# Optimization experiments

Measured on AMD Instinct MI355X. Metric: run time of the kernel, lower is better.

## Reference

```python
import jax, jax.numpy as jnp
import numpy as np
from jax import lax

N_EMBED, N_HEAD, N_EXPERTS, TOP_K = 1024, 16, 8, 2
D_FF = 4 * N_EMBED
HEAD = N_EMBED // N_HEAD
LN_EPS = 1e-5


def _layernorm(x, gamma, beta):
    mu = jnp.mean(x, axis=-1, keepdims=True)
    var = jnp.var(x, axis=-1, keepdims=True)
    return (x - mu) * lax.rsqrt(var + LN_EPS) * gamma + beta


def setup_inputs() -> dict:
    key = jax.random.key(0)
    ks = jax.random.split(key, 16)
    B, T = 2, 2048
    s = 0.02
    return {
        "x": jax.random.normal(ks[0], (B, T, N_EMBED), jnp.float32),
        "noise": jax.random.normal(ks[1], (B, T, N_EXPERTS), jnp.float32),
        "gamma1": jnp.ones((N_EMBED,), jnp.float32),
        "beta1": jnp.zeros((N_EMBED,), jnp.float32),
        "gamma2": jnp.ones((N_EMBED,), jnp.float32),
        "beta2": jnp.zeros((N_EMBED,), jnp.float32),
        "w_qkv": jax.random.normal(ks[2], (N_EMBED, 3 * N_EMBED), jnp.float32) * s,
        "w_out": jax.random.normal(ks[3], (N_EMBED, N_EMBED), jnp.float32) * s,
        "w_route": jax.random.normal(ks[4], (N_EMBED, N_EXPERTS), jnp.float32) * s,
        "b_route": jnp.zeros((N_EXPERTS,), jnp.float32),
        "w_noise": jax.random.normal(ks[5], (N_EMBED, N_EXPERTS), jnp.float32) * s,
        "b_noise": jnp.zeros((N_EXPERTS,), jnp.float32),
        "w1": jax.random.normal(ks[6], (N_EXPERTS, N_EMBED, D_FF), jnp.float32) * s,
        "b1": jnp.zeros((N_EXPERTS, D_FF), jnp.float32),
        "w2": jax.random.normal(ks[7], (N_EXPERTS, D_FF, N_EMBED), jnp.float32) * s,
        "b2": jnp.zeros((N_EXPERTS, N_EMBED), jnp.float32),
    }


def _attention(h, w_qkv, w_out):
    B, T, C = h.shape
    qkv = (h @ w_qkv).reshape(B, T, 3, N_HEAD, HEAD)
    q, k, v = qkv[:, :, 0], qkv[:, :, 1], qkv[:, :, 2]  # (B,T,H,hd)
    scores = jnp.einsum("bthd,bshd->bhts", q, k) / jnp.sqrt(jnp.float32(HEAD))
    attn = jax.nn.softmax(scores, axis=-1)
    out = jnp.einsum("bhts,bshd->bthd", attn, v)  # (B,T,H,hd)
    # faithful reproduction of the original permute/reshape/permute sequence
    out = jnp.transpose(out, (0, 2, 1, 3)).reshape(B, C, T)
    out = jnp.transpose(out, (0, 2, 1))  # (B,T,C)
    return out @ w_out


def _sparse_moe(h, noise, w_route, b_route, w_noise, b_noise, w1, b1, w2, b2):
    B, T, C = h.shape
    N = B * T
    flat = h.reshape(N, C)
    logits = flat @ w_route + b_route
    noise_logits = flat @ w_noise + b_noise
    noisy = logits + noise.reshape(N, N_EXPERTS) * jax.nn.softplus(noise_logits)
    full_probs = jax.nn.softmax(noisy, axis=-1)
    top_vals, top_idx = lax.top_k(noisy, TOP_K)  # (N,k)
    gates = jax.nn.softmax(top_vals, axis=-1)
    dense_gates = jnp.zeros((N, N_EXPERTS), flat.dtype).at[
        jnp.arange(N)[:, None], top_idx
    ].set(gates)
    cap = (N * TOP_K) // N_EXPERTS  # expert capacity, capacity_factor=1.0
    updates = jnp.zeros_like(flat)
    for i in range(N_EXPERTS):
        mask = (top_idx == i).any(axis=-1)  # (N,)
        order = jnp.argsort((~mask).astype(jnp.int32), stable=True)
        idx = order[:cap]
        valid = mask[idx]
        xi = flat[idx]  # (cap,C)
        hid = jax.nn.relu(xi @ w1[i] + b1[i])
        yo = hid @ w2[i] + b2[i]
        g = dense_gates[idx, i] * valid.astype(flat.dtype)
        updates = updates.at[idx].add(yo * g[:, None])
    moe_out = updates.reshape(B, T, C)
    entropy = -jnp.sum(full_probs * jnp.log(full_probs + 1e-8), axis=-1)
    return moe_out, entropy.mean()


def reference(x, noise, gamma1, beta1, gamma2, beta2, w_qkv, w_out,
              w_route, b_route, w_noise, b_noise, w1, b1, w2, b2):
    x = x + _attention(_layernorm(x, gamma1, beta1), w_qkv, w_out)
    moe_out, entropy_loss = _sparse_moe(_layernorm(x, gamma2, beta2), noise,
                                        w_route, b_route, w_noise, b_noise,
                                        w1, b1, w2, b2)
    return x + moe_out, entropy_loss
```

## Files before the change

kernel.cpp:

```cpp
#include <hip/hip_runtime.h>
#include <hip/hip_bf16.h>


#define TT   2048
#define NTOK 4096
#define CE   1024
#define DFF  4096
#define NE   8
#define CAP  1024

typedef __bf16 bf16;
typedef __attribute__((ext_vector_type(8))) bf16 bf16x8;
typedef __attribute__((ext_vector_type(4))) bf16 bf16x4;
typedef __attribute__((ext_vector_type(4))) float f32x4;

typedef __attribute__((address_space(1))) const void* as1_t;
typedef __attribute__((address_space(3))) void* as3_t;
__device__ __forceinline__ void gll16(const void* g, void* l) {
  __builtin_amdgcn_global_load_lds((as1_t)g, (as3_t)l, 16, 0, 0);
}

__device__ __forceinline__ void split2(float v, bf16& h, bf16& l) {
  h = (bf16)v;
  l = (bf16)(v - (float)h);
}

template <bool LO>
__global__ __launch_bounds__(256) void wsplit_k(const float* __restrict__ W,
                                                bf16* __restrict__ Th,
                                                bf16* __restrict__ Tl,
                                                int K, int N, long sW, long sT) {
  __shared__ float tile[64][65];
  const int e = blockIdx.z;
  const float* Wb = W + (long)e * sW;
  bf16* Thb = Th + (long)e * sT;
  bf16* Tlb = LO ? Tl + (long)e * sT : nullptr;
  const int k0 = blockIdx.y * 64, n0 = blockIdx.x * 64;
  const int tx = threadIdx.x & 15, ty = threadIdx.x >> 4;
#pragma unroll
  for (int i = 0; i < 4; i++) {
    int kk = ty + i * 16;
    float4 v = *(const float4*)&Wb[(long)(k0 + kk) * N + n0 + tx * 4];
    tile[kk][tx * 4 + 0] = v.x;
    tile[kk][tx * 4 + 1] = v.y;
    tile[kk][tx * 4 + 2] = v.z;
    tile[kk][tx * 4 + 3] = v.w;
  }
  __syncthreads();
#pragma unroll
  for (int i = 0; i < 4; i++) {
    int nn = ty + i * 16;
    bf16x4 hv, lv;
#pragma unroll
    for (int j = 0; j < 4; j++) {
      float v = tile[tx * 4 + j][nn];
      bf16 h, l;
      split2(v, h, l);
      hv[j] = h;
      lv[j] = l;
    }
    long o = (long)(n0 + nn) * K + k0 + tx * 4;
    *(bf16x4*)(Thb + o) = hv;
    if (LO) *(bf16x4*)(Tlb + o) = lv;
  }
}

__global__ __launch_bounds__(256) void vsplit_k(const float* __restrict__ V,
                                                bf16* __restrict__ Th,
                                                bf16* __restrict__ Tl) {
  __shared__ float tile[64][65];
  const int b = blockIdx.z;
  const int vd0 = blockIdx.x * 64, t0 = blockIdx.y * 64;
  const int tx = threadIdx.x & 15, ty = threadIdx.x >> 4;
#pragma unroll
  for (int i = 0; i < 4; i++) {
    int tt = ty + i * 16;
    float4 v = *(const float4*)&V[((long)b * TT + t0 + tt) * 1024 + vd0 + tx * 4];
    tile[tt][tx * 4 + 0] = v.x;
    tile[tt][tx * 4 + 1] = v.y;
    tile[tt][tx * 4 + 2] = v.z;
    tile[tt][tx * 4 + 3] = v.w;
  }
  __syncthreads();
#pragma unroll
  for (int i = 0; i < 4; i++) {
    int vd = ty + i * 16;
    bf16x4 hv, lv;
#pragma unroll
    for (int j = 0; j < 4; j++) {
      float v = tile[tx * 4 + j][vd];
      bf16 h, l;
      split2(v, h, l);
      hv[j] = h;
      lv[j] = l;
    }
    long o = ((long)b * 1024 + vd0 + vd) * (long)TT + t0 + tx * 4;
    *(bf16x4*)(Th + o) = hv;
    *(bf16x4*)(Tl + o) = lv;
  }
}

__global__ __launch_bounds__(256) void ln_k(const float* __restrict__ in,
                                            const float* __restrict__ g,
                                            const float* __restrict__ b,
                                            float* __restrict__ outf,
                                            bf16* __restrict__ outh,
                                            bf16* __restrict__ outl,
                                            float* __restrict__ zp) {
  int row = blockIdx.x, tid = threadIdx.x;
  if (zp && row == 0 && tid < 64) zp[tid] = 0.f;
  const float* xr = in + (long)row * CE;
  float v[4];
  float s = 0.f, s2 = 0.f;
#pragma unroll
  for (int i = 0; i < 4; i++) {
    v[i] = xr[tid + 256 * i];
    s += v[i];
    s2 += v[i] * v[i];
  }
#pragma unroll
  for (int o = 32; o; o >>= 1) {
    s += __shfl_xor(s, o);
    s2 += __shfl_xor(s2, o);
  }
  __shared__ float rs[4], rs2[4];
  int w = tid >> 6, lane = tid & 63;
  if (lane == 0) { rs[w] = s; rs2[w] = s2; }
  __syncthreads();
  s = rs[0] + rs[1] + rs[2] + rs[3];
  s2 = rs2[0] + rs2[1] + rs2[2] + rs2[3];
  float mu = s * (1.f / CE);
  float var = s2 * (1.f / CE) - mu * mu;
  float rstd = rsqrtf(var + 1e-5f);
  long rb = (long)row * CE;
#pragma unroll
  for (int i = 0; i < 4; i++) {
    int c = tid + 256 * i;
    float y = (v[i] - mu) * rstd * g[c] + b[c];
    if (outf) outf[rb + c] = y;
    bf16 h, l;
    split2(y, h, l);
    outh[rb + c] = h;
    outl[rb + c] = l;
  }
}

template <int NPASS, int EPI, bool AGATHER, int TM>
__global__ __launch_bounds__(256, 2) void gemm_k(
    const bf16* __restrict__ Ah, const bf16* __restrict__ Al,
    const bf16* __restrict__ BTh, const bf16* __restrict__ BTl,
    void* __restrict__ O0, void* __restrict__ O1, void* __restrict__ O2,
    int M, int N, int K, const float* __restrict__ resid,
    const float* __restrict__ bias, const int* __restrict__ tokens,
    const int* __restrict__ counts, const float* __restrict__ gslot,
    long sA, long sBT, long sC, int sBias, const bf16* __restrict__ zp) {
  constexpr int NS = (NPASS > 1) ? 2 : 1;
  constexpr int MI = TM / 32;
  constexpr int AISS = TM / 64;
  __shared__ bf16 As[NS][TM * 32];
  __shared__ bf16 Bs[NS][128 * 32];
  const int e = blockIdx.z;
  const int n0 = blockIdx.x * 128, m0 = blockIdx.y * TM;
  const int tid = threadIdx.x;
  const int w = tid >> 6, lane = tid & 63, lm = lane & 15, qd = lane >> 4;
  const int wm = (w & 1) * (TM / 2), wn = (w >> 1) * 64;

  const bf16* Ab = Ah + (long)e * sA;
  const bf16* AbL = (NS > 1) ? Al + (long)e * sA : nullptr;
  const bf16* Bb = BTh + (long)e * sBT;
  const bf16* BbL = (NS > 1) ? BTl + (long)e * sBT : nullptr;

  const int kc = (lane & 3) * 8;
  int cnt = 0;
  if (AGATHER || EPI == 3) cnt = counts[e];

  const bf16* aP[AISS];
  const bf16* aPL[AISS];
  int aStep[AISS];
  int ldsA[AISS];
#pragma unroll
  for (int ii = 0; ii < AISS; ii++) {
    int sr = w * (TM / 4) + ii * 16 + (lane >> 2);
    ldsA[ii] = (w * TM + ii * 64) * 8;
    aStep[ii] = 32;
    if (AGATHER) {
      int gm = m0 + sr;
      int tk = (gm < cnt) ? tokens[e * CAP + gm] : -1;
      if (tk < 0) { aP[ii] = (const bf16*)zp + kc; aStep[ii] = 0; }
      else aP[ii] = Ab + (long)tk * K + kc;
    } else {
      aP[ii] = Ab + (long)(m0 + sr) * K + kc;
    }
    aPL[ii] = (NS > 1) ? AbL + (aP[ii] - Ab) : nullptr;
  }
  const bf16* bP[2];
  const bf16* bPL[2];
  int ldsB[2];
#pragma unroll
  for (int ii = 0; ii < 2; ii++) {
    int sr = w * 32 + ii * 16 + (lane >> 2);
    ldsB[ii] = (w * 128 + ii * 64) * 8;
    bP[ii] = Bb + (long)(n0 + sr) * K + kc;
    bPL[ii] = (NS > 1) ? BbL + (bP[ii] - Bb) : nullptr;
  }

  f32x4 acc[MI][4];
#pragma unroll
  for (int i = 0; i < MI; i++)
#pragma unroll
    for (int j = 0; j < 4; j++) acc[i][j] = (f32x4){0.f, 0.f, 0.f, 0.f};

  for (int k0 = 0; k0 < K; k0 += 32) {
#pragma unroll
    for (int ii = 0; ii < AISS; ii++) {
      gll16(aP[ii], (char*)&As[0][0] + ldsA[ii] * 2);
      if (NS > 1) gll16(aPL[ii], (char*)&As[1][0] + ldsA[ii] * 2);
      aP[ii] += aStep[ii];
      if (NS > 1) aPL[ii] += aStep[ii];
    }
#pragma unroll
    for (int ii = 0; ii < 2; ii++) {
      gll16(bP[ii], (char*)&Bs[0][0] + ldsB[ii] * 2);
      if (NS > 1) gll16(bPL[ii], (char*)&Bs[1][0] + ldsB[ii] * 2);
      bP[ii] += 32;
      if (NS > 1) bPL[ii] += 32;
    }
    __syncthreads();
    bf16x8 af[NS][MI], bfv[NS][4];
#pragma unroll
    for (int j = 0; j < 4; j++)
#pragma unroll
      for (int s = 0; s < NS; s++)
        bfv[s][j] = *(const bf16x8*)&Bs[s][(wn + j * 16 + lm) * 32 + qd * 8];
#pragma unroll
    for (int i = 0; i < MI; i++)
#pragma unroll
      for (int s = 0; s < NS; s++)
        af[s][i] = *(const bf16x8*)&As[s][(wm + i * 16 + lm) * 32 + qd * 8];
#pragma unroll
    for (int i = 0; i < MI; i++)
#pragma unroll
      for (int j = 0; j < 4; j++) {
        acc[i][j] = __builtin_amdgcn_mfma_f32_16x16x32_bf16(
            af[0][i], bfv[0][j], acc[i][j], 0, 0, 0);
        if (NPASS > 1) {
          acc[i][j] = __builtin_amdgcn_mfma_f32_16x16x32_bf16(
              af[0][i], bfv[1][j], acc[i][j], 0, 0, 0);
          acc[i][j] = __builtin_amdgcn_mfma_f32_16x16x32_bf16(
              af[1][i], bfv[0][j], acc[i][j], 0, 0, 0);
        }
      }
    __syncthreads();
  }
#pragma unroll
  for (int i = 0; i < MI; i++)
#pragma unroll
    for (int j = 0; j < 4; j++) {
      long row = m0 + wm + i * 16 + qd * 4;
      long col = n0 + wn + j * 16 + lm;
      if (EPI == 0) {
        if (col < 2048) {
          bf16* qh = (bf16*)O0;
          bf16* ql = (bf16*)O1;
#pragma unroll
          for (int r = 0; r < 4; r++) {
            bf16 h, l;
            split2(acc[i][j][r], h, l);
            qh[(row + r) * 2048 + col] = h;
            ql[(row + r) * 2048 + col] = l;
          }
        } else {
          float* vt = (float*)O2;
          long vd = col - 2048;
#pragma unroll
          for (int r = 0; r < 4; r++) vt[(row + r) * 1024 + vd] = acc[i][j][r];
        }
      } else if (EPI == 1) {
        float* outp = (float*)O0;
#pragma unroll
        for (int r = 0; r < 4; r++)
          outp[(row + r) * N + col] = resid[(row + r) * N + col] + acc[i][j][r];
      } else if (EPI == 2) {
        bf16* hid = (bf16*)O0;
        float bv = bias[e * sBias + col];
#pragma unroll
        for (int r = 0; r < 4; r++) {
          float t = acc[i][j][r] + bv;
          hid[(long)e * sC + (row + r) * (long)N + col] =
              (bf16)(t > 0.f ? t : 0.f);
        }
      } else {
        float* outp = (float*)O0;
        float bv = bias[e * sBias + col];
#pragma unroll
        for (int r = 0; r < 4; r++) {
          long rr = row + r;
          if (rr < cnt) {
            int tok = tokens[e * CAP + rr];
            float gv = gslot[e * CAP + rr];
            atomicAdd(&outp[(long)tok * CE + col], gv * (acc[i][j][r] + bv));
          }
        }
      }
    }
}

__global__ __launch_bounds__(512, 4) void attn_k(
    const bf16* __restrict__ qkvh, const bf16* __restrict__ qkvl,
    const bf16* __restrict__ VTh, const bf16* __restrict__ VTl,
    bf16* __restrict__ attn_h, bf16* __restrict__ attn_l) {
  const int qt = blockIdx.x, h = blockIdx.y, b = blockIdx.z;
  const int tid = threadIdx.x, w = tid >> 6, lane = tid & 63;
  const int lm = lane & 15, qd = lane >> 4;
  __shared__ bf16 Ks[2][64 * 64];
  __shared__ bf16 Vs[2][64 * 64];
  __shared__ bf16 Ps[8][2][16][40];
  const long bb = (long)b * TT;

  bf16x8 qfh[2], qfl[2];
  {
    long qrow = (bb + qt * 128 + w * 16 + lm) * 2048 + h * 64;
#pragma unroll
    for (int kk = 0; kk < 2; kk++) {
      qfh[kk] = *(const bf16x8*)(qkvh + qrow + kk * 32 + qd * 8);
      qfl[kk] = *(const bf16x8*)(qkvl + qrow + kk * 32 + qd * 8);
    }
  }

  const int ktok = tid >> 3, dc = tid & 7;
  const int kws = ktok * 64 + ((dc ^ (ktok & 7)) * 8);
  const long gK0 = (bb + ktok) * 2048 + 1024 + h * 64 + dc * 8;
  const int vd = tid >> 3, tc = tid & 7;
  const int vws = vd * 64 + ((tc ^ (vd & 7)) * 8);
  const long gV0 = ((long)b * 1024 + h * 64 + vd) * (long)TT + tc * 8;

  const bf16* pKh = qkvh + gK0;
  const bf16* pKl = qkvl + gK0;
  const bf16* pVh = VTh + gV0;
  const bf16* pVl = VTl + gV0;

  float4 rkh, rkl, rvh, rvl;
#define LOADT()                  \
  do {                           \
    rkh = *(const float4*)(pKh); \
    rkl = *(const float4*)(pKl); \
    rvh = *(const float4*)(pVh); \
    rvl = *(const float4*)(pVl); \
  } while (0)
  LOADT();

  float l_lane[4];
  f32x4 o[4];
#pragma unroll
  for (int r = 0; r < 4; r++) l_lane[r] = 0.f;
#pragma unroll
  for (int nt = 0; nt < 4; nt++) o[nt] = (f32x4){0.f, 0.f, 0.f, 0.f};

  const float SC = 0.125f * 1.4426950408889634f;

  for (int kt = 0; kt < TT / 64; kt++) {
    __syncthreads();
    *(float4*)&Ks[0][kws] = rkh;
    *(float4*)&Ks[1][kws] = rkl;
    *(float4*)&Vs[0][vws] = rvh;
    *(float4*)&Vs[1][vws] = rvl;
    if (kt != TT / 64 - 1) {
      pKh += 64 * 2048; pKl += 64 * 2048; pVh += 64; pVl += 64;
      LOADT();
    }
    __syncthreads();
#pragma unroll
    for (int th = 0; th < 2; th++) {
      f32x4 sv[2];
#pragma unroll
      for (int ntl = 0; ntl < 2; ntl++) sv[ntl] = (f32x4){0.f, 0.f, 0.f, 0.f};
#pragma unroll
      for (int ntl = 0; ntl < 2; ntl++) {
        int tok = (th * 2 + ntl) * 16 + lm;
#pragma unroll
        for (int kk = 0; kk < 2; kk++) {
          int slot = ((kk * 4 + qd) ^ (lm & 7)) * 8;
          bf16x8 kh = *(const bf16x8*)&Ks[0][tok * 64 + slot];
          bf16x8 kl = *(const bf16x8*)&Ks[1][tok * 64 + slot];
          sv[ntl] = __builtin_amdgcn_mfma_f32_16x16x32_bf16(qfh[kk], kh,
                                                            sv[ntl], 0, 0, 0);
          sv[ntl] = __builtin_amdgcn_mfma_f32_16x16x32_bf16(qfh[kk], kl,
                                                            sv[ntl], 0, 0, 0);
          sv[ntl] = __builtin_amdgcn_mfma_f32_16x16x32_bf16(qfl[kk], kh,
                                                            sv[ntl], 0, 0, 0);
        }
      }
#pragma unroll
      for (int ntl = 0; ntl < 2; ntl++)
#pragma unroll
        for (int r = 0; r < 4; r++) {
          float p = __builtin_exp2f(sv[ntl][r] * SC);
          l_lane[r] += p;
          bf16 hh, ll;
          split2(p, hh, ll);
          Ps[w][0][qd * 4 + r][ntl * 16 + lm] = hh;
          Ps[w][1][qd * 4 + r][ntl * 16 + lm] = ll;
        }
      bf16x8 ph = *(const bf16x8*)&Ps[w][0][lm][qd * 8];
      bf16x8 pl = *(const bf16x8*)&Ps[w][1][lm][qd * 8];
#pragma unroll
      for (int nt = 0; nt < 4; nt++) {
        int drow = nt * 16 + lm;
        int slot = ((th * 4 + qd) ^ (lm & 7)) * 8;
        bf16x8 vh = *(const bf16x8*)&Vs[0][drow * 64 + slot];
        bf16x8 vl = *(const bf16x8*)&Vs[1][drow * 64 + slot];
        o[nt] = __builtin_amdgcn_mfma_f32_16x16x32_bf16(ph, vh, o[nt], 0, 0, 0);
        o[nt] = __builtin_amdgcn_mfma_f32_16x16x32_bf16(ph, vl, o[nt], 0, 0, 0);
        o[nt] = __builtin_amdgcn_mfma_f32_16x16x32_bf16(pl, vh, o[nt], 0, 0, 0);
      }
    }
  }
#pragma unroll
  for (int r = 0; r < 4; r++)
#pragma unroll
    for (int d = 8; d; d >>= 1) l_lane[r] += __shfl_xor(l_lane[r], d);
#pragma unroll
  for (int nt = 0; nt < 4; nt++)
#pragma unroll
    for (int r = 0; r < 4; r++) {
      int t = qt * 128 + w * 16 + qd * 4 + r;
      int d = nt * 16 + lm;
      int ttn = (t & 31) * 64 + d;
      int c = h * 64 + (t >> 5);
      float v = o[nt][r] / l_lane[r];
      bf16 hh, ll;
      split2(v, hh, ll);
      long idx = (bb + ttn) * (long)CE + c;
      attn_h[idx] = hh;
      attn_l[idx] = ll;
    }
#undef LOADT
}

__global__ __launch_bounds__(64) void route_k(
    const float* __restrict__ hln, const float* __restrict__ noise,
    const float* __restrict__ wr, const float* __restrict__ br,
    const float* __restrict__ wn, const float* __restrict__ bn,
    int* __restrict__ top_e, float* __restrict__ gates,
    float* __restrict__ entb) {
  int n = blockIdx.x, lane = threadIdx.x;
  const float* hr = hln + (long)n * CE;
  float aR[NE], aN[NE];
#pragma unroll
  for (int e = 0; e < NE; e++) { aR[e] = 0.f; aN[e] = 0.f; }
  for (int i = lane; i < CE; i += 64) {
    float hv = hr[i];
#pragma unroll
    for (int e = 0; e < NE; e++) {
      aR[e] += hv * wr[i * NE + e];
      aN[e] += hv * wn[i * NE + e];
    }
  }
#pragma unroll
  for (int e = 0; e < NE; e++)
#pragma unroll
    for (int d = 32; d; d >>= 1) {
      aR[e] += __shfl_xor(aR[e], d);
      aN[e] += __shfl_xor(aN[e], d);
    }
  if (lane == 0) {
    float ns[NE];
#pragma unroll
    for (int e = 0; e < NE; e++) {
      float lg = aR[e] + br[e];
      float nl = aN[e] + bn[e];
      float sp = (nl > 20.f) ? nl : log1pf(expf(nl));
      ns[e] = lg + noise[(long)n * NE + e] * sp;
    }
    int i0 = 0;
#pragma unroll
    for (int e = 1; e < NE; e++)
      if (ns[e] > ns[i0]) i0 = e;
    int i1 = (i0 == 0) ? 1 : 0;
#pragma unroll
    for (int e = 0; e < NE; e++)
      if (e != i0 && ns[e] > ns[i1]) i1 = e;
    float v0 = ns[i0], v1 = ns[i1];
    float e1v = expf(v1 - v0);
    float inv2 = 1.f / (1.f + e1v);
    top_e[2 * n] = i0;
    top_e[2 * n + 1] = i1;
    gates[2 * n] = inv2;
    gates[2 * n + 1] = e1v * inv2;
    float ssum = 0.f, p[NE];
#pragma unroll
    for (int e = 0; e < NE; e++) {
      p[e] = expf(ns[e] - v0);
      ssum += p[e];
    }
    float is = 1.f / ssum, ent = 0.f;
#pragma unroll
    for (int e = 0; e < NE; e++) {
      float pe = p[e] * is;
      ent -= pe * logf(pe + 1e-8f);
    }
    entb[n] = ent;
  }
}

__global__ __launch_bounds__(256) void assign_k(const int* __restrict__ top_e,
                                                const float* __restrict__ gates,
                                                int* __restrict__ tokens,
                                                float* __restrict__ gslot,
                                                int* __restrict__ counts) {
  int e = blockIdx.x, tid = threadIdx.x, w = tid >> 6, lane = tid & 63;
  __shared__ int wtot[4];
  int basec = 0;
  for (int c = 0; c < 16; c++) {
    int n = c * 256 + tid;
    int e0 = top_e[2 * n], e1 = top_e[2 * n + 1];
    bool flag = (e0 == e) || (e1 == e);
    int rank = (e0 == e) ? 0 : 1;
    unsigned long long mask = __ballot(flag);
    int pre = __popcll(mask & ((1ull << lane) - 1ull));
    if (lane == 0) wtot[w] = __popcll(mask);
    __syncthreads();
    int wbase = basec;
    for (int i = 0; i < w; i++) wbase += wtot[i];
    if (flag) {
      int slot = wbase + pre;
      if (slot < CAP) {
        tokens[e * CAP + slot] = n;
        gslot[e * CAP + slot] = gates[2 * n + rank];
      }
    }
    int tot = wtot[0] + wtot[1] + wtot[2] + wtot[3];
    __syncthreads();
    basec += tot;
  }
  if (tid == 0) counts[e] = basec < CAP ? basec : CAP;
}

__global__ __launch_bounds__(256) void entropy_k(const float* __restrict__ entb,
                                                 float* __restrict__ outp) {
  int tid = threadIdx.x;
  float s = 0.f;
  for (int i = tid; i < NTOK; i += 256) s += entb[i];
#pragma unroll
  for (int d = 32; d; d >>= 1) s += __shfl_xor(s, d);
  __shared__ float rs[4];
  int w = tid >> 6, lane = tid & 63;
  if (lane == 0) rs[w] = s;
  __syncthreads();
  if (tid == 0)
    outp[(long)NTOK * CE] = (rs[0] + rs[1] + rs[2] + rs[3]) * (1.f / NTOK);
}

extern "C" void kernel_launch(void* const* d_in, const int* in_sizes, int n_in,
                              void* d_out, int out_size, void* d_ws,
                              size_t ws_size, hipStream_t stream) {
  const float* x = (const float*)d_in[0];
  const float* noise = (const float*)d_in[1];
  const float* gamma1 = (const float*)d_in[2];
  const float* beta1 = (const float*)d_in[3];
  const float* gamma2 = (const float*)d_in[4];
  const float* beta2 = (const float*)d_in[5];
  const float* w_qkv = (const float*)d_in[6];
  const float* w_out = (const float*)d_in[7];
  const float* w_route = (const float*)d_in[8];
  const float* b_route = (const float*)d_in[9];
  const float* w_noise = (const float*)d_in[10];
  const float* b_noise = (const float*)d_in[11];
  const float* w1 = (const float*)d_in[12];
  const float* b1 = (const float*)d_in[13];
  const float* w2 = (const float*)d_in[14];
  const float* b2 = (const float*)d_in[15];
  float* out = (float*)d_out;

  char* ws = (char*)d_ws;
  size_t offA = 0;
  bf16* qkvh = (bf16*)(ws + offA);  offA += (size_t)NTOK * 2048 * 2;
  bf16* qkvl = (bf16*)(ws + offA);  offA += (size_t)NTOK * 2048 * 2;
  bf16* VTh = (bf16*)(ws + offA);   offA += (size_t)2 * 1024 * TT * 2;
  bf16* VTl = (bf16*)(ws + offA);   offA += (size_t)2 * 1024 * TT * 2;
  size_t attn_off = offA;
  bf16* attn_h = (bf16*)(ws + offA); offA += (size_t)NTOK * CE * 2;
  bf16* attn_l = (bf16*)(ws + offA); offA += (size_t)NTOK * CE * 2;
  bf16* hid = (bf16*)ws;
  float* vtmp = (float*)(ws + attn_off);
  float* h2f = (float*)(ws + attn_off);
  size_t szA = offA;
  size_t offB = szA;
  bf16* h1h = (bf16*)(ws + offB);    offB += (size_t)NTOK * CE * 2;
  bf16* h1l = (bf16*)(ws + offB);    offB += (size_t)NTOK * CE * 2;
  bf16* wqkvTh = (bf16*)(ws + offB); offB += (size_t)3072 * 1024 * 2;
  bf16* wqkvTl = (bf16*)(ws + offB); offB += (size_t)3072 * 1024 * 2;
  bf16* woutTh = (bf16*)(ws + offB); offB += (size_t)1024 * 1024 * 2;
  bf16* woutTl = (bf16*)(ws + offB); offB += (size_t)1024 * 1024 * 2;
  bf16* h2h = (bf16*)(ws + szA);
  bf16* h2l = (bf16*)(ws + szA + (size_t)NTOK * CE * 2);
  size_t offC = offB;
  bf16* w1T = (bf16*)(ws + offC);
  bf16* w2T = w1T;
  offC += (size_t)NE * DFF * CE * 2;
  size_t offS = offC;
  int* top_e = (int*)(ws + offS);    offS += (size_t)NTOK * 2 * 4;
  float* gates = (float*)(ws + offS); offS += (size_t)NTOK * 2 * 4;
  int* toks = (int*)(ws + offS);     offS += (size_t)NE * CAP * 4;
  float* gslot = (float*)(ws + offS); offS += (size_t)NE * CAP * 4;
  int* counts = (int*)(ws + offS);   offS += 256;
  float* entb = (float*)(ws + offS); offS += (size_t)NTOK * 4;
  float* zp = (float*)(ws + offS);   offS += 256;
  if (offS > ws_size) return;

  wsplit_k<true><<<dim3(48, 16, 1), 256, 0, stream>>>(w_qkv, wqkvTh, wqkvTl,
                                                      1024, 3072, 0, 0);
  wsplit_k<true><<<dim3(16, 16, 1), 256, 0, stream>>>(w_out, woutTh, woutTl,
                                                      1024, 1024, 0, 0);
  wsplit_k<false><<<dim3(64, 16, 8), 256, 0, stream>>>(
      w1, w1T, nullptr, 1024, DFF, (long)CE * DFF, (long)DFF * CE);
  ln_k<<<NTOK, 256, 0, stream>>>(x, gamma1, beta1, nullptr, h1h, h1l, zp);
  gemm_k<3, 0, false, 128><<<dim3(24, 32, 1), 256, 0, stream>>>(
      h1h, h1l, wqkvTh, wqkvTl, qkvh, qkvl, vtmp, NTOK, 3 * CE, CE, nullptr,
      nullptr, nullptr, nullptr, nullptr, 0, 0, 0, 0, (const bf16*)zp);
  vsplit_k<<<dim3(16, 32, 2), 256, 0, stream>>>(vtmp, VTh, VTl);
  attn_k<<<dim3(16, 16, 2), 512, 0, stream>>>(qkvh, qkvl, VTh, VTl, attn_h,
                                              attn_l);
  gemm_k<3, 1, false, 64><<<dim3(8, 64, 1), 256, 0, stream>>>(
      attn_h, attn_l, woutTh, woutTl, out, nullptr, nullptr, NTOK, CE, CE, x,
      nullptr, nullptr, nullptr, nullptr, 0, 0, 0, 0, (const bf16*)zp);
  ln_k<<<NTOK, 256, 0, stream>>>(out, gamma2, beta2, h2f, h2h, h2l, nullptr);
  route_k<<<NTOK, 64, 0, stream>>>(h2f, noise, w_route, b_route, w_noise,
                                   b_noise, top_e, gates, entb);
  assign_k<<<NE, 256, 0, stream>>>(top_e, gates, toks, gslot, counts);
  gemm_k<1, 2, true, 128><<<dim3(DFF / 128, CAP / 128, NE), 256, 0, stream>>>(
      h2h, nullptr, w1T, nullptr, hid, nullptr, nullptr, CAP, DFF, CE, nullptr,
      b1, toks, counts, nullptr, 0, (long)DFF * CE, (long)CAP * DFF, DFF,
      (const bf16*)zp);
  wsplit_k<false><<<dim3(16, 64, 8), 256, 0, stream>>>(
      w2, w2T, nullptr, DFF, CE, (long)DFF * CE, (long)CE * DFF);
  gemm_k<1, 3, false, 128><<<dim3(CE / 128, CAP / 128, NE), 256, 0, stream>>>(
      hid, nullptr, w2T, nullptr, out, nullptr, nullptr, CAP, CE, DFF, nullptr,
      b2, toks, counts, gslot, (long)CAP * DFF, (long)CE * DFF, 0, CE,
      (const bf16*)zp);
  entropy_k<<<1, 256, 0, stream>>>(entb, out);
}
```

Measured before the change: 909.7 us.

## Double-buffer 32-token K/V tiles in attention with split hi/lo loaders

The attention kernel now streams K and V in 32-token tiles into two LDS buffers, so each iteration needs one barrier instead of two. The loading work is split: half the threads load the high bf16 parts and the other half load the low parts. The QK dot product is split into two independent accumulators to shorten MFMA dependency chains, and s_setprio raises wave priority around the MFMA bursts. This aims to overlap global loads with compute and cut barrier stalls, at the cost of smaller tiles and twice as many loop iterations.

```diff
diff --git a/kernel.cpp b/kernel.cpp
--- a/kernel.cpp
+++ b/kernel.cpp
@@ -312,8 +312,8 @@
   const int qt = blockIdx.x, h = blockIdx.y, b = blockIdx.z;
   const int tid = threadIdx.x, w = tid >> 6, lane = tid & 63;
   const int lm = lane & 15, qd = lane >> 4;
-  __shared__ bf16 Ks[2][64 * 64];
-  __shared__ bf16 Vs[2][64 * 64];
+  __shared__ bf16 Ks[2][2][32 * 64];
+  __shared__ bf16 Vs[2][2][64 * 32];
   __shared__ bf16 Ps[8][2][16][40];
   const long bb = (long)b * TT;
 
@@ -327,27 +327,16 @@
     }
   }
 
-  const int ktok = tid >> 3, dc = tid & 7;
-  const int kws = ktok * 64 + ((dc ^ (ktok & 7)) * 8);
-  const long gK0 = (bb + ktok) * 2048 + 1024 + h * 64 + dc * 8;
-  const int vd = tid >> 3, tc = tid & 7;
-  const int vws = vd * 64 + ((tc ^ (vd & 7)) * 8);
-  const long gV0 = ((long)b * 1024 + h * 64 + vd) * (long)TT + tc * 8;
-
-  const bf16* pKh = qkvh + gK0;
-  const bf16* pKl = qkvl + gK0;
-  const bf16* pVh = VTh + gV0;
-  const bf16* pVl = VTl + gV0;
-
-  float4 rkh, rkl, rvh, rvl;
-#define LOADT()                  \
-  do {                           \
-    rkh = *(const float4*)(pKh); \
-    rkl = *(const float4*)(pKl); \
-    rvh = *(const float4*)(pVh); \
-    rvl = *(const float4*)(pVl); \
-  } while (0)
-  LOADT();
+  const int sH = (tid < 256) ? 0 : 1;
+  const int si = tid & 255;
+  const int ktok = si >> 3, kdc = si & 7;
+  const int kws = ktok * 64 + ((kdc ^ (ktok & 7)) * 8);
+  const long gK = (bb + ktok) * 2048L + 1024 + h * 64 + kdc * 8;
+  const int vd = si >> 2, vtc = si & 3;
+  const int vws = vd * 32 + ((vtc ^ (vd & 3)) * 8);
+  const long gV = ((long)b * 1024 + h * 64 + vd) * (long)TT + vtc * 8;
+  const bf16* pK = (sH ? qkvl : qkvh) + gK;
+  const bf16* pV = (sH ? VTl : VTh) + gV;
 
   float l_lane[4];
   f32x4 o[4];
@@ -357,64 +346,84 @@
   for (int nt = 0; nt < 4; nt++) o[nt] = (f32x4){0.f, 0.f, 0.f, 0.f};
 
   const float SC = 0.125f * 1.4426950408889634f;
-
-  for (int kt = 0; kt < TT / 64; kt++) {
+  const int NT = TT / 32;
+
+  auto compute = [&](int cb) {
+    f32x4 svA[2], svB[2];
+#pragma unroll
+    for (int ntl = 0; ntl < 2; ntl++) {
+      svA[ntl] = (f32x4){0.f, 0.f, 0.f, 0.f};
+      svB[ntl] = (f32x4){0.f, 0.f, 0.f, 0.f};
+    }
+    __builtin_amdgcn_s_setprio(1);
+#pragma unroll
+    for (int ntl = 0; ntl < 2; ntl++) {
+      int tok = ntl * 16 + lm;
+      int sw = lm & 7;
+      bf16x8 kh0 = *(const bf16x8*)&Ks[cb][0][tok * 64 + ((qd ^ sw) * 8)];
+      bf16x8 kl0 = *(const bf16x8*)&Ks[cb][1][tok * 64 + ((qd ^ sw) * 8)];
+      bf16x8 kh1 = *(const bf16x8*)&Ks[cb][0][tok * 64 + (((4 + qd) ^ sw) * 8)];
+      bf16x8 kl1 = *(const bf16x8*)&Ks[cb][1][tok * 64 + (((4 + qd) ^ sw) * 8)];
+      svA[ntl] = __builtin_amdgcn_mfma_f32_16x16x32_bf16(qfh[0], kh0, svA[ntl], 0, 0, 0);
+      svA[ntl] = __builtin_amdgcn_mfma_f32_16x16x32_bf16(qfh[0], kl0, svA[ntl], 0, 0, 0);
+      svA[ntl] = __builtin_amdgcn_mfma_f32_16x16x32_bf16(qfl[0], kh0, svA[ntl], 0, 0, 0);
+      svB[ntl] = __builtin_amdgcn_mfma_f32_16x16x32_bf16(qfh[1], kh1, svB[ntl], 0, 0, 0);
+      svB[ntl] = __builtin_amdgcn_mfma_f32_16x16x32_bf16(qfh[1], kl1, svB[ntl], 0, 0, 0);
+      svB[ntl] = __builtin_amdgcn_mfma_f32_16x16x32_bf16(qfl[1], kh1, svB[ntl], 0, 0, 0);
+    }
+    __builtin_amdgcn_s_setprio(0);
+#pragma unroll
+    for (int ntl = 0; ntl < 2; ntl++)
+#pragma unroll
+      for (int r = 0; r < 4; r++) {
+        float p = __builtin_exp2f((svA[ntl][r] + svB[ntl][r]) * SC);
+        l_lane[r] += p;
+        bf16 hh, ll;
+        split2(p, hh, ll);
+        Ps[w][0][qd * 4 + r][ntl * 16 + lm] = hh;
+        Ps[w][1][qd * 4 + r][ntl * 16 + lm] = ll;
+      }
+    bf16x8 ph = *(const bf16x8*)&Ps[w][0][lm][qd * 8];
+    bf16x8 pl = *(const bf16x8*)&Ps[w][1][lm][qd * 8];
+    __builtin_amdgcn_s_setprio(1);
+#pragma unroll
+    for (int nt = 0; nt < 4; nt++) {
+      int drow = nt * 16 + lm;
+      int slot = ((qd ^ (lm & 3)) * 8);
+      bf16x8 vh = *(const bf16x8*)&Vs[cb][0][drow * 32 + slot];
+      bf16x8 vl = *(const bf16x8*)&Vs[cb][1][drow * 32 + slot];
+      o[nt] = __builtin_amdgcn_mfma_f32_16x16x32_bf16(ph, vh, o[nt], 0, 0, 0);
+      o[nt] = __builtin_amdgcn_mfma_f32_16x16x32_bf16(ph, vl, o[nt], 0, 0, 0);
+      o[nt] = __builtin_amdgcn_mfma_f32_16x16x32_bf16(pl, vh, o[nt], 0, 0, 0);
+    }
+    __builtin_amdgcn_s_setprio(0);
+  };
+
+  float4 rkA = *(const float4*)(pK);
+  float4 rvA = *(const float4*)(pV);
+  float4 rkB, rvB;
+
+  for (int kt = 0; kt < NT; kt += 2) {
+    *(float4*)&Ks[0][sH][kws] = rkA;
+    *(float4*)&Vs[0][sH][vws] = rvA;
+    {
+      long okt = (long)(kt + 1);
+      rkB = *(const float4*)(pK + okt * (32L * 2048));
+      rvB = *(const float4*)(pV + okt * 32);
+    }
     __syncthreads();
-    *(float4*)&Ks[0][kws] = rkh;
-    *(float4*)&Ks[1][kws] = rkl;
-    *(float4*)&Vs[0][vws] = rvh;
-    *(float4*)&Vs[1][vws] = rvl;
-    if (kt != TT / 64 - 1) {
-      pKh += 64 * 2048; pKl += 64 * 2048; pVh += 64; pVl += 64;
-      LOADT();
+    compute(0);
+    *(float4*)&Ks[1][sH][kws] = rkB;
+    *(float4*)&Vs[1][sH][vws] = rvB;
+    if (kt + 2 < NT) {
+      long okt = (long)(kt + 2);
+      rkA = *(const float4*)(pK + okt * (32L * 2048));
+      rvA = *(const float4*)(pV + okt * 32);
     }
     __syncthreads();
-#pragma unroll
-    for (int th = 0; th < 2; th++) {
-      f32x4 sv[2];
-#pragma unroll
-      for (int ntl = 0; ntl < 2; ntl++) sv[ntl] = (f32x4){0.f, 0.f, 0.f, 0.f};
-#pragma unroll
-      for (int ntl = 0; ntl < 2; ntl++) {
-        int tok = (th * 2 + ntl) * 16 + lm;
-#pragma unroll
-        for (int kk = 0; kk < 2; kk++) {
-          int slot = ((kk * 4 + qd) ^ (lm & 7)) * 8;
-          bf16x8 kh = *(const bf16x8*)&Ks[0][tok * 64 + slot];
-          bf16x8 kl = *(const bf16x8*)&Ks[1][tok * 64 + slot];
-          sv[ntl] = __builtin_amdgcn_mfma_f32_16x16x32_bf16(qfh[kk], kh,
-                                                            sv[ntl], 0, 0, 0);
-          sv[ntl] = __builtin_amdgcn_mfma_f32_16x16x32_bf16(qfh[kk], kl,
-                                                            sv[ntl], 0, 0, 0);
-          sv[ntl] = __builtin_amdgcn_mfma_f32_16x16x32_bf16(qfl[kk], kh,
-                                                            sv[ntl], 0, 0, 0);
-        }
-      }
-#pragma unroll
-      for (int ntl = 0; ntl < 2; ntl++)
-#pragma unroll
-        for (int r = 0; r < 4; r++) {
-          float p = __builtin_exp2f(sv[ntl][r] * SC);
-          l_lane[r] += p;
-          bf16 hh, ll;
-          split2(p, hh, ll);
-          Ps[w][0][qd * 4 + r][ntl * 16 + lm] = hh;
-          Ps[w][1][qd * 4 + r][ntl * 16 + lm] = ll;
-        }
-      bf16x8 ph = *(const bf16x8*)&Ps[w][0][lm][qd * 8];
-      bf16x8 pl = *(const bf16x8*)&Ps[w][1][lm][qd * 8];
-#pragma unroll
-      for (int nt = 0; nt < 4; nt++) {
-        int drow = nt * 16 + lm;
-        int slot = ((th * 4 + qd) ^ (lm & 7)) * 8;
-        bf16x8 vh = *(const bf16x8*)&Vs[0][drow * 64 + slot];
-        bf16x8 vl = *(const bf16x8*)&Vs[1][drow * 64 + slot];
-        o[nt] = __builtin_amdgcn_mfma_f32_16x16x32_bf16(ph, vh, o[nt], 0, 0, 0);
-        o[nt] = __builtin_amdgcn_mfma_f32_16x16x32_bf16(ph, vl, o[nt], 0, 0, 0);
-        o[nt] = __builtin_amdgcn_mfma_f32_16x16x32_bf16(pl, vh, o[nt], 0, 0, 0);
-      }
-    }
-  }
+    compute(1);
+  }
+
 #pragma unroll
   for (int r = 0; r < 4; r++)
 #pragma unroll
@@ -434,7 +443,6 @@
       attn_h[idx] = hh;
       attn_l[idx] = ll;
     }
-#undef LOADT
 }
 
 __global__ __launch_bounds__(64) void route_k(
```

New measurement: 933.2 us. +2.6%, slower.
